# Kernel tuning notes

Measured on AMD Instinct MI355X. Metric: run time of the kernel, lower is better.

The kernel has to match this reference:

```python
import jax, jax.numpy as jnp
import numpy as np

B, S, D_IN, E, H = 2, 2048, 1024, 1024, 16  # batch, seq, input_size, embedding_size, heads


def setup_inputs() -> dict:
    key = jax.random.key(0)
    k1, k2, k3 = jax.random.split(key, 3)
    x = jax.random.normal(k1, (B, S, D_IN), dtype=jnp.float32)
    # fused QKV projection weight stored as [in, 3E] (torch Linear weight transposed)
    W0 = jax.random.normal(k2, (D_IN, 3 * E), dtype=jnp.float32) * (1.0 / np.sqrt(D_IN))
    b0 = jax.random.normal(k3, (3 * E,), dtype=jnp.float32) * 0.02
    return {"x": x, "W0": W0, "b0": b0}


def reference(x, W0, b0):
    b, s, _ = x.shape
    y = x @ W0 + b0                              # [B,S,3E]
    y = y.reshape(b, s, H, -1).transpose(0, 2, 1, 3)  # [B,H,S,3*head_dim]
    q, k, v = jnp.split(y, 3, axis=-1)           # each [B,H,S,head_dim]
    scale = 1.0 / jnp.sqrt(jnp.asarray(D_IN, dtype=x.dtype))  # NB: sqrt(input_size), as in source
    scores = jnp.einsum("bhqd,bhkd->bhqk", q, k) * scale
    # causal mask: -inf above diagonal
    causal = jnp.triu(jnp.full((s, s), -jnp.inf, dtype=scores.dtype), k=1)
    scores = scores + causal
    attn = jax.nn.softmax(scores, axis=-1)       # [B,H,S,S]
    o = jnp.einsum("bhqk,bhkd->bhqd", attn, v)   # [B,H,S,head_dim]
    # faithful to source: reshape directly from (B,H,S,d) to (B,S,H*d) WITHOUT permuting back
    return o.reshape(b, s, -1)
```

## Files before the change

### kernel.cpp

```cpp
#include <hip/hip_runtime.h>
#include <stdint.h>

typedef __attribute__((ext_vector_type(4))) float f32x4;
typedef __attribute__((ext_vector_type(16))) float f32x16;
typedef __attribute__((ext_vector_type(8))) short bf16x8;
typedef __attribute__((ext_vector_type(4))) short bf16x4;

#define MFMA16(a, b, c) __builtin_amdgcn_mfma_f32_16x16x32_bf16((a), (b), (c), 0, 0, 0)
#define MFMA32(a, b, c) __builtin_amdgcn_mfma_f32_32x32x16_bf16((a), (b), (c), 0, 0, 0)

__device__ __forceinline__ short f2bf(float f) {
    union { float f; uint32_t u; } v; v.f = f;
    uint32_t r = (v.u + 0x7fffu + ((v.u >> 16) & 1u)) >> 16;
    return (short)(uint16_t)r;
}
__device__ __forceinline__ float bf2f(short s) {
    union { uint32_t u; float f; } v; v.u = ((uint32_t)(uint16_t)s) << 16;
    return v.f;
}
__device__ __forceinline__ float fast_exp2(float x) {
    float r; asm("v_exp_f32 %0, %1" : "=v"(r) : "v"(x)); return r;
}

__device__ __forceinline__ void async_ld16(const short* g, short* l) {
    __builtin_amdgcn_global_load_lds(
        (const __attribute__((address_space(1))) uint32_t*)g,
        (__attribute__((address_space(3))) uint32_t*)l, 16, 0, 0);
}

#define MK_BFRAG(C, O, OUT) do {                                                   \
    uint32_t a_, b_, c_, d_;                                                       \
    asm("v_cvt_pk_bf16_f32 %0, %1, %2" : "=v"(a_) : "v"((C)[(O)+0]), "v"((C)[(O)+1])); \
    asm("v_cvt_pk_bf16_f32 %0, %1, %2" : "=v"(c_) : "v"((C)[(O)+2]), "v"((C)[(O)+3])); \
    asm("v_cvt_pk_bf16_f32 %0, %1, %2" : "=v"(b_) : "v"((C)[(O)+4]), "v"((C)[(O)+5])); \
    asm("v_cvt_pk_bf16_f32 %0, %1, %2" : "=v"(d_) : "v"((C)[(O)+6]), "v"((C)[(O)+7])); \
    asm("v_permlane32_swap_b32 %0, %1" : "+v"(a_), "+v"(b_));                      \
    asm("v_permlane32_swap_b32 %0, %1" : "+v"(c_), "+v"(d_));                      \
    union { uint32_t u[4]; bf16x8 v; } pb_;                                        \
    pb_.u[0] = a_; pb_.u[1] = c_; pb_.u[2] = b_; pb_.u[3] = d_;                    \
    OUT = pb_.v;                                                                   \
} while (0)

__global__ __launch_bounds__(256)
void convert_fused(const float* __restrict__ X, short* __restrict__ Xb,
                   const float* __restrict__ W, short* __restrict__ Wt) {
    __shared__ short T[64][72];
    const int t = threadIdx.x;
    const int id = blockIdx.x;
    if (id < 2048) {
        const int i8 = (id * 256 + t) << 3;
        f32x4 a = *(const f32x4*)(X + i8);
        f32x4 b = *(const f32x4*)(X + i8 + 4);
        bf16x8 o;
#pragma unroll
        for (int j = 0; j < 4; ++j) { o[j] = f2bf(a[j]); o[4 + j] = f2bf(b[j]); }
        *(bf16x8*)(Xb + i8) = o;
        return;
    }
    const int wid = id - 2048;
    const int n0 = (wid % 48) * 64, k0 = (wid / 48) * 64;
#pragma unroll
    for (int i = 0; i < 4; ++i) {
        const int r = i * 16 + (t >> 4);
        const int c = (t & 15) << 2;
        f32x4 v = *(const f32x4*)(W + (size_t)(k0 + r) * 3072 + n0 + c);
#pragma unroll
        for (int j = 0; j < 4; ++j) T[c + j][r] = f2bf(v[j]);
    }
    __syncthreads();
#pragma unroll
    for (int i = 0; i < 2; ++i) {
        const int r = i * 32 + (t >> 3);
        const int c = (t & 7) << 3;
        *(bf16x8*)(Wt + (size_t)(n0 + r) * 1024 + k0 + c) = *(const bf16x8*)&T[r][c];
    }
}

__global__ __launch_bounds__(256, 3)
void gemm_pack(const short* __restrict__ Xb, const short* __restrict__ Wt,
               const float* __restrict__ bias, short* __restrict__ Qp,
               short* __restrict__ Kp, short* __restrict__ Vp) {
    __shared__ short Asm[3][128 * 32];
    __shared__ short Bsm[3][128 * 32];

    const int tid  = threadIdx.x;
    const int lane = tid & 63;
    const int l15  = lane & 15;
    const int lq   = lane >> 4;
    const int wave = tid >> 6;
    const int wr = wave >> 1, wc = wave & 1;

    const int bid = blockIdx.x;
    const int swz = (bid & 7) * 96 + (bid >> 3);
    const int m0 = (swz / 24) * 128, n0 = (swz % 24) * 128;

    const int srow = tid >> 2;
    const int scolsw = (((tid & 3) ^ (srow & 3)) << 3);

    f32x4 acc[4][4];
#pragma unroll
    for (int m = 0; m < 4; ++m)
#pragma unroll
        for (int n = 0; n < 4; ++n) acc[m][n] = (f32x4)(0.0f);

    auto stage = [&](int k0, int bb) {
#pragma unroll
        for (int i = 0; i < 2; ++i)
            async_ld16(Xb + (size_t)(m0 + i * 64 + srow) * 1024 + k0 + scolsw,
                       &Asm[bb][(i * 256 + wave * 64) * 8]);
#pragma unroll
        for (int i = 0; i < 2; ++i)
            async_ld16(Wt + (size_t)(n0 + i * 64 + srow) * 1024 + k0 + scolsw,
                       &Bsm[bb][(i * 256 + wave * 64) * 8]);
    };

    const int gsw = ((lq ^ (l15 & 3)) << 3);

    auto compute = [&](int bb) {
        bf16x8 af[4], bfv[4];
#pragma unroll
        for (int m = 0; m < 4; ++m)
            af[m] = *(const bf16x8*)&Asm[bb][(wr * 64 + m * 16 + l15) * 32 + gsw];
#pragma unroll
        for (int n = 0; n < 4; ++n)
            bfv[n] = *(const bf16x8*)&Bsm[bb][(wc * 64 + n * 16 + l15) * 32 + gsw];
#pragma unroll
        for (int m = 0; m < 4; ++m)
#pragma unroll
            for (int n = 0; n < 4; ++n) acc[m][n] = MFMA16(af[m], bfv[n], acc[m][n]);
    };

#define WAITV(N) do {                                           \
        asm volatile("s_waitcnt vmcnt(" #N ")" ::: "memory");   \
        __builtin_amdgcn_sched_barrier(0);                      \
        __builtin_amdgcn_s_barrier();                           \
        __builtin_amdgcn_sched_barrier(0);                      \
    } while (0)

    stage(0, 0);
    stage(32, 1);
#pragma unroll 1
    for (int kt = 0; kt < 30; ++kt) {
        WAITV(4);
        compute(kt % 3);
        stage((kt + 2) * 32, (kt + 2) % 3);
    }
    WAITV(4);
    compute(0);
    WAITV(0);
    compute(1);
#undef WAITV

    const float SCALE2 = 0.03125f * 1.44269504f;
    float bv[4];
#pragma unroll
    for (int n = 0; n < 4; ++n) bv[n] = bias[n0 + wc * 64 + n * 16 + l15];

    const size_t bbase = (size_t)(m0 >> 11) * 2097152;
    const int tokb = (m0 & 2047) + wr * 64;

#pragma unroll
    for (int n = 0; n < 4; ++n) {
        const int col = n0 + wc * 64 + n * 16 + l15;
        const int h   = col / 192;
        const int seg = (col >> 6) % 3;
        const int d   = col & 63;
        const size_t hb = bbase + (size_t)h * 131072;
        if (seg == 0) {
            const int cp = ((d >> 4) << 9) + (((d >> 3) & 1) << 8) + (d & 7);
#pragma unroll
            for (int m = 0; m < 4; ++m)
#pragma unroll
                for (int r = 0; r < 4; ++r) {
                    const int tok = tokb + m * 16 + (lq << 2) + r;
                    Qp[hb + ((size_t)(tok >> 5) << 11) + ((tok & 31) << 3) + cp] =
                        f2bf((acc[m][n][r] + bv[n]) * SCALE2);
                }
        } else if (seg == 1) {
            const int cp = ((d >> 4) << 10) + (((d >> 3) & 1) << 8) + (d & 7);
#pragma unroll
            for (int m = 0; m < 4; ++m)
#pragma unroll
                for (int r = 0; r < 4; ++r) {
                    const int tok = tokb + m * 16 + (lq << 2) + r;
                    Kp[hb + ((size_t)(tok >> 6) << 12) + (((tok >> 5) & 1) << 9)
                       + ((tok & 31) << 3) + cp] = f2bf(acc[m][n][r] + bv[n]);
                }
        } else {
            const int cp = ((d >> 5) << 11) + ((d & 31) << 3);
#pragma unroll
            for (int m = 0; m < 4; ++m)
#pragma unroll
                for (int r = 0; r < 4; ++r) {
                    const int tok = tokb + m * 16 + (lq << 2) + r;
                    Vp[hb + ((size_t)(tok >> 6) << 12) + (((tok >> 4) & 3) << 9)
                       + (((tok >> 3) & 1) << 8) + (tok & 7) + cp] =
                        f2bf(acc[m][n][r] + bv[n]);
                }
        }
    }
}

__global__ __launch_bounds__(64, 3)
void attn_part(const short* __restrict__ Qp, const short* __restrict__ Kp,
               const short* __restrict__ Vp, short* __restrict__ Po,
               float* __restrict__ Pm) {
    const int tid = threadIdx.x;
    const int l31 = tid & 31;
    const int hi  = tid >> 5;

    const int id  = blockIdx.x;
    const int xcd = id & 7;
    const int idx = id >> 3;
    const int u   = idx >> 2;
    const int bh  = xcd * 4 + (idx & 3);

    int qt, t0, t1;
    bool hasDiag;
    if (u < 32) {
        qt = u + 32; t0 = 0; t1 = 16; hasDiag = false;
    } else {
        const int s = 16 - ((u - 32) >> 2);
        const int j = (u - 32) & 3;
        if (j < 2) { qt = 2 * s - 2 + j;       t0 = 0;  t1 = s; }
        else       { qt = 2 * s + 30 + (j - 2); t0 = 16; t1 = s + 16; }
        hasDiag = true;
    }
    const int q0 = qt * 32;

    const size_t hb = (size_t)bh * 131072;

    bf16x8 qf[4];
    {
        const short* qp = Qp + hb + qt * 2048 + tid * 8;
#pragma unroll
        for (int dg = 0; dg < 4; ++dg) qf[dg] = *(const bf16x8*)(qp + dg * 512);
    }

    f32x16 o0 = (f32x16)(0.f), o1 = (f32x16)(0.f);
    float m_run = -1e30f, l_run = 0.f;
    const int qg = q0 + l31;

    bf16x8 kA[8], kB[8], va[8];

    auto loadK = [&](bf16x8 (&kr)[8], int t) {
        const short* p = Kp + hb + (size_t)t * 4096 + tid * 8;
#pragma unroll
        for (int f = 0; f < 8; ++f)
            kr[f] = *(const bf16x8*)(p + (f >> 1) * 1024 + (f & 1) * 512);
    };
    auto loadV = [&](int t) {
        const short* p = Vp + hb + (size_t)t * 4096 + tid * 8;
#pragma unroll
        for (int f = 0; f < 8; ++f) va[f] = *(const bf16x8*)(p + f * 512);
    };
    auto qk = [&](bf16x8 (&kr)[8], f32x16& c0, f32x16& c1) {
#pragma unroll
        for (int dg = 0; dg < 4; ++dg) {
            c0 = MFMA32(kr[2 * dg],     qf[dg], c0);
            c1 = MFMA32(kr[2 * dg + 1], qf[dg], c1);
        }
    };

    auto smpv = [&](f32x16& c0, f32x16& c1, int kv0, bool DIAG) {
        if (DIAG) {
#pragma unroll
            for (int r = 0; r < 16; ++r) {
                const int kvr = kv0 + (r & 3) + 8 * (r >> 2) + 4 * hi;
                if (kvr > qg)      c0[r] = -1e30f;
                if (kvr + 32 > qg) c1[r] = -1e30f;
            }
        }

        float mr[8];
#pragma unroll
        for (int r = 0; r < 8; ++r)
            mr[r] = fmaxf(fmaxf(c0[r], c0[8 + r]), fmaxf(c1[r], c1[8 + r]));
        float mx = fmaxf(fmaxf(fmaxf(mr[0], mr[1]), fmaxf(mr[2], mr[3])),
                         fmaxf(fmaxf(mr[4], mr[5]), fmaxf(mr[6], mr[7])));
        mx = fmaxf(mx, __shfl_xor(mx, 32, 64));

        if (!__all(mx <= m_run + 8.f)) {
            const float mnew = fmaxf(m_run, mx);
            const float corr = fast_exp2(m_run - mnew);
            l_run *= corr;
            o0 = o0 * corr;
            o1 = o1 * corr;
            m_run = mnew;
        }

        float ps0 = 0.f, ps1 = 0.f, ps2 = 0.f, ps3 = 0.f;
#pragma unroll
        for (int r = 0; r < 4; ++r) {
            c0[r]      = fast_exp2(c0[r]      - m_run); ps0 += c0[r];
            c0[4 + r]  = fast_exp2(c0[4 + r]  - m_run); ps1 += c0[4 + r];
            c0[8 + r]  = fast_exp2(c0[8 + r]  - m_run); ps2 += c0[8 + r];
            c0[12 + r] = fast_exp2(c0[12 + r] - m_run); ps3 += c0[12 + r];
        }
#pragma unroll
        for (int r = 0; r < 4; ++r) {
            c1[r]      = fast_exp2(c1[r]      - m_run); ps0 += c1[r];
            c1[4 + r]  = fast_exp2(c1[4 + r]  - m_run); ps1 += c1[4 + r];
            c1[8 + r]  = fast_exp2(c1[8 + r]  - m_run); ps2 += c1[8 + r];
            c1[12 + r] = fast_exp2(c1[12 + r] - m_run); ps3 += c1[12 + r];
        }
        l_run += (ps0 + ps1) + (ps2 + ps3);

        bf16x8 bf00, bf01, bf10, bf11;
        MK_BFRAG(c0, 0, bf00);
        MK_BFRAG(c0, 8, bf01);
        MK_BFRAG(c1, 0, bf10);
        MK_BFRAG(c1, 8, bf11);

        o0 = MFMA32(va[0], bf00, o0);
        o0 = MFMA32(va[1], bf01, o0);
        o0 = MFMA32(va[2], bf10, o0);
        o0 = MFMA32(va[3], bf11, o0);
        o1 = MFMA32(va[4], bf00, o1);
        o1 = MFMA32(va[5], bf01, o1);
        o1 = MFMA32(va[6], bf10, o1);
        o1 = MFMA32(va[7], bf11, o1);
    };

    int t = t0;
    loadK(kA, t0);
#pragma unroll 1
    for (; t + 2 < t1; t += 2) {
        f32x16 c0 = (f32x16)(0.f), c1 = (f32x16)(0.f);
        qk(kA, c0, c1);
        loadK(kB, t + 1);
        loadV(t);
        smpv(c0, c1, t * 64, false);
        f32x16 d0 = (f32x16)(0.f), d1 = (f32x16)(0.f);
        qk(kB, d0, d1);
        loadK(kA, t + 2);
        loadV(t + 1);
        smpv(d0, d1, (t + 1) * 64, false);
    }
    if (t + 1 < t1) {
        f32x16 c0 = (f32x16)(0.f), c1 = (f32x16)(0.f);
        qk(kA, c0, c1);
        loadK(kB, t + 1);
        loadV(t);
        smpv(c0, c1, t * 64, false);
        f32x16 d0 = (f32x16)(0.f), d1 = (f32x16)(0.f);
        qk(kB, d0, d1);
        loadV(t + 1);
        smpv(d0, d1, (t + 1) * 64, hasDiag);
    } else {
        f32x16 c0 = (f32x16)(0.f), c1 = (f32x16)(0.f);
        qk(kA, c0, c1);
        loadV(t);
        smpv(c0, c1, t * 64, hasDiag);
    }

    const float l_tot = l_run + __shfl_xor(l_run, 32, 64);
    const float inv = 1.f / l_tot;
    const int prow = (bh * 96 + u) * 32 + l31;
#pragma unroll
    for (int g = 0; g < 4; ++g) {
        bf16x4 w4;
#pragma unroll
        for (int j = 0; j < 4; ++j) w4[j] = f2bf(o0[g * 4 + j] * inv);
        *(bf16x4*)&Po[(size_t)prow * 64 + 8 * g + 4 * hi] = w4;
#pragma unroll
        for (int j = 0; j < 4; ++j) w4[j] = f2bf(o1[g * 4 + j] * inv);
        *(bf16x4*)&Po[(size_t)prow * 64 + 32 + 4 * hi + 8 * g] = w4;
    }
    if (hi == 0) Pm[prow] = m_run + __log2f(l_tot);
}

__global__ __launch_bounds__(256)
void attn_combine(const short* __restrict__ Po, const float* __restrict__ Pm,
                  float* __restrict__ Out) {
    const int idx = blockIdx.x * 256 + threadIdx.x;
    const int d4 = (idx & 15) << 2;
    const int rg = idx >> 4;
    const int q  = rg & 2047;
    const int bh = rg >> 11;
    const int qt = q >> 5, r = q & 31;

    f32x4 ov;
    if (qt < 32) {
        const int s = (qt >> 1) + 1;
        const int u = 32 + (16 - s) * 4 + (qt & 1);
        const int p0 = (bh * 96 + u) * 32 + r;
        bf16x4 a = *(const bf16x4*)&Po[(size_t)p0 * 64 + d4];
#pragma unroll
        for (int j = 0; j < 4; ++j) ov[j] = bf2f(a[j]);
    } else {
        const int u0 = qt - 32;
        const int s  = (qt >> 1) - 15;
        const int u1 = 32 + (16 - s) * 4 + 2 + (qt & 1);
        const int p0 = (bh * 96 + u0) * 32 + r;
        const int p1 = (bh * 96 + u1) * 32 + r;
        bf16x4 a = *(const bf16x4*)&Po[(size_t)p0 * 64 + d4];
        bf16x4 c = *(const bf16x4*)&Po[(size_t)p1 * 64 + d4];
        const float m0 = Pm[p0], m1 = Pm[p1];
        const float M = fmaxf(m0, m1);
        const float w0 = exp2f(m0 - M), w1 = exp2f(m1 - M);
        const float inv = 1.f / (w0 + w1);
#pragma unroll
        for (int j = 0; j < 4; ++j) ov[j] = (w0 * bf2f(a[j]) + w1 * bf2f(c[j])) * inv;
    }
    *(f32x4*)&Out[(size_t)rg * 64 + d4] = ov;
}

extern "C" void kernel_launch(void* const* d_in, const int* in_sizes, int n_in,
                              void* d_out, int out_size, void* d_ws, size_t ws_size,
                              hipStream_t stream) {
    const float* x  = (const float*)d_in[0];
    const float* W0 = (const float*)d_in[1];
    const float* b0 = (const float*)d_in[2];
    float* out = (float*)d_out;
    char* ws = (char*)d_ws;

    const size_t SEG_B = (size_t)32 * 131072 * 2;
    const size_t QKV_B = 3 * SEG_B;
    const size_t XBF_B = (size_t)4096 * 1024 * 2;
    const size_t PO_B  = (size_t)32 * 96 * 32 * 64 * 2;

    short* qp = (short*)ws;
    short* kp = (short*)(ws + SEG_B);
    short* vp = (short*)(ws + 2 * SEG_B);
    short* xb = (short*)(ws + QKV_B);
    short* wt = (short*)(ws + QKV_B + XBF_B);
    short* po = (short*)(ws + QKV_B);
    float* pm = (float*)(ws + QKV_B + PO_B);

    convert_fused<<<dim3(2816), dim3(256), 0, stream>>>(x, xb, W0, wt);
    gemm_pack<<<dim3(768), dim3(256), 0, stream>>>(xb, wt, b0, qp, kp, vp);
    attn_part<<<dim3(3072), dim3(64), 0, stream>>>(qp, kp, vp, po, pm);
    attn_combine<<<dim3(4096), dim3(256), 0, stream>>>(po, pm, out);
}
```

Before: 87.64 us.

## Split attention KV loop across four waves with LDS softmax merge

Each attention block now runs four wavefronts instead of one. The waves take interleaved KV tiles (stride 4), and their partial outputs and max/sum statistics are merged through shared memory with a log-sum-exp rescale by wave 0. The goal is to cut per-block serial latency over the KV loop and raise the number of in-flight waves. In exchange it adds a barrier, LDS traffic and combine arithmetic. Waves with no tiles sit idle for short diagonal tiles, and the register budget under launch bounds 256 may tighten.

Measured after the change: 147.8 us. +68.6%, slower.

```diff
diff --git a/kernel.cpp b/kernel.cpp
--- a/kernel.cpp
+++ b/kernel.cpp
@@ -201,13 +201,18 @@
     }
 }
 
-__global__ __launch_bounds__(64, 3)
+__global__ __launch_bounds__(256, 3)
 void attn_part(const short* __restrict__ Qp, const short* __restrict__ Kp,
                const short* __restrict__ Vp, short* __restrict__ Po,
                float* __restrict__ Pm) {
-    const int tid = threadIdx.x;
-    const int l31 = tid & 31;
-    const int hi  = tid >> 5;
+    __shared__ float oX[3][32 * 65];
+    __shared__ float lmX[3][64];
+
+    const int tid  = threadIdx.x;
+    const int lane = tid & 63;
+    const int l31  = tid & 31;
+    const int hi   = (tid >> 5) & 1;
+    const int w    = tid >> 6;
 
     const int id  = blockIdx.x;
     const int xcd = id & 7;
@@ -216,23 +221,22 @@
     const int bh  = xcd * 4 + (idx & 3);
 
     int qt, t0, t1;
-    bool hasDiag;
     if (u < 32) {
-        qt = u + 32; t0 = 0; t1 = 16; hasDiag = false;
+        qt = u + 32; t0 = 0; t1 = 16;
     } else {
         const int s = 16 - ((u - 32) >> 2);
         const int j = (u - 32) & 3;
-        if (j < 2) { qt = 2 * s - 2 + j;       t0 = 0;  t1 = s; }
+        if (j < 2) { qt = 2 * s - 2 + j;        t0 = 0;  t1 = s; }
         else       { qt = 2 * s + 30 + (j - 2); t0 = 16; t1 = s + 16; }
-        hasDiag = true;
     }
     const int q0 = qt * 32;
+    const int dt = qt >> 1;
 
     const size_t hb = (size_t)bh * 131072;
 
     bf16x8 qf[4];
     {
-        const short* qp = Qp + hb + qt * 2048 + tid * 8;
+        const short* qp = Qp + hb + qt * 2048 + lane * 8;
 #pragma unroll
         for (int dg = 0; dg < 4; ++dg) qf[dg] = *(const bf16x8*)(qp + dg * 512);
     }
@@ -244,13 +248,13 @@
     bf16x8 kA[8], kB[8], va[8];
 
     auto loadK = [&](bf16x8 (&kr)[8], int t) {
-        const short* p = Kp + hb + (size_t)t * 4096 + tid * 8;
+        const short* p = Kp + hb + (size_t)t * 4096 + lane * 8;
 #pragma unroll
         for (int f = 0; f < 8; ++f)
             kr[f] = *(const bf16x8*)(p + (f >> 1) * 1024 + (f & 1) * 512);
     };
     auto loadV = [&](int t) {
-        const short* p = Vp + hb + (size_t)t * 4096 + tid * 8;
+        const short* p = Vp + hb + (size_t)t * 4096 + lane * 8;
 #pragma unroll
         for (int f = 0; f < 8; ++f) va[f] = *(const bf16x8*)(p + f * 512);
     };
@@ -322,52 +326,102 @@
         o1 = MFMA32(va[7], bf11, o1);
     };
 
-    int t = t0;
-    loadK(kA, t0);
+    int t = t0 + w;
+    if (t < t1) {
+        loadK(kA, t);
 #pragma unroll 1
-    for (; t + 2 < t1; t += 2) {
-        f32x16 c0 = (f32x16)(0.f), c1 = (f32x16)(0.f);
-        qk(kA, c0, c1);
-        loadK(kB, t + 1);
-        loadV(t);
-        smpv(c0, c1, t * 64, false);
-        f32x16 d0 = (f32x16)(0.f), d1 = (f32x16)(0.f);
-        qk(kB, d0, d1);
-        loadK(kA, t + 2);
-        loadV(t + 1);
-        smpv(d0, d1, (t + 1) * 64, false);
-    }
-    if (t + 1 < t1) {
-        f32x16 c0 = (f32x16)(0.f), c1 = (f32x16)(0.f);
-        qk(kA, c0, c1);
-        loadK(kB, t + 1);
-        loadV(t);
-        smpv(c0, c1, t * 64, false);
-        f32x16 d0 = (f32x16)(0.f), d1 = (f32x16)(0.f);
-        qk(kB, d0, d1);
-        loadV(t + 1);
-        smpv(d0, d1, (t + 1) * 64, hasDiag);
-    } else {
-        f32x16 c0 = (f32x16)(0.f), c1 = (f32x16)(0.f);
-        qk(kA, c0, c1);
-        loadV(t);
-        smpv(c0, c1, t * 64, hasDiag);
+        while (t + 8 < t1) {
+            f32x16 c0 = (f32x16)(0.f), c1 = (f32x16)(0.f);
+            qk(kA, c0, c1);
+            loadK(kB, t + 4);
+            loadV(t);
+            smpv(c0, c1, t * 64, t == dt);
+            f32x16 d0 = (f32x16)(0.f), d1 = (f32x16)(0.f);
+            qk(kB, d0, d1);
+            loadK(kA, t + 8);
+            loadV(t + 4);
+            smpv(d0, d1, (t + 4) * 64, (t + 4) == dt);
+            t += 8;
+        }
+        if (t + 4 < t1) {
+            f32x16 c0 = (f32x16)(0.f), c1 = (f32x16)(0.f);
+            qk(kA, c0, c1);
+            loadK(kB, t + 4);
+            loadV(t);
+            smpv(c0, c1, t * 64, t == dt);
+            f32x16 d0 = (f32x16)(0.f), d1 = (f32x16)(0.f);
+            qk(kB, d0, d1);
+            loadV(t + 4);
+            smpv(d0, d1, (t + 4) * 64, (t + 4) == dt);
+        } else {
+            f32x16 c0 = (f32x16)(0.f), c1 = (f32x16)(0.f);
+            qk(kA, c0, c1);
+            loadV(t);
+            smpv(c0, c1, t * 64, t == dt);
+        }
     }
 
     const float l_tot = l_run + __shfl_xor(l_run, 32, 64);
-    const float inv = 1.f / l_tot;
-    const int prow = (bh * 96 + u) * 32 + l31;
-#pragma unroll
-    for (int g = 0; g < 4; ++g) {
-        bf16x4 w4;
-#pragma unroll
-        for (int j = 0; j < 4; ++j) w4[j] = f2bf(o0[g * 4 + j] * inv);
-        *(bf16x4*)&Po[(size_t)prow * 64 + 8 * g + 4 * hi] = w4;
-#pragma unroll
-        for (int j = 0; j < 4; ++j) w4[j] = f2bf(o1[g * 4 + j] * inv);
-        *(bf16x4*)&Po[(size_t)prow * 64 + 32 + 4 * hi + 8 * g] = w4;
-    }
-    if (hi == 0) Pm[prow] = m_run + __log2f(l_tot);
+
+    if (w > 0) {
+        float* dst = &oX[w - 1][l31 * 65];
+#pragma unroll
+        for (int g = 0; g < 4; ++g) {
+            f32x4 v0, v1;
+#pragma unroll
+            for (int j = 0; j < 4; ++j) { v0[j] = o0[4 * g + j]; v1[j] = o1[4 * g + j]; }
+            *(f32x4*)&dst[8 * g + 4 * hi]      = v0;
+            *(f32x4*)&dst[32 + 8 * g + 4 * hi] = v1;
+        }
+        if (hi == 0) { lmX[w - 1][l31 * 2] = m_run; lmX[w - 1][l31 * 2 + 1] = l_tot; }
+    }
+    __syncthreads();
+
+    if (w == 0) {
+        float mw[3], lw[3];
+        float M = m_run;
+#pragma unroll
+        for (int i = 0; i < 3; ++i) {
+            mw[i] = lmX[i][l31 * 2];
+            lw[i] = lmX[i][l31 * 2 + 1];
+            M = fmaxf(M, mw[i]);
+        }
+        const float wt0 = fast_exp2(m_run - M);
+        float L = l_tot * wt0;
+        float wts[3];
+#pragma unroll
+        for (int i = 0; i < 3; ++i) { wts[i] = fast_exp2(mw[i] - M); L += lw[i] * wts[i]; }
+
+        f32x16 a0 = o0 * wt0, a1 = o1 * wt0;
+#pragma unroll
+        for (int i = 0; i < 3; ++i) {
+            const float* src = &oX[i][l31 * 65];
+#pragma unroll
+            for (int g = 0; g < 4; ++g) {
+                f32x4 v0 = *(const f32x4*)&src[8 * g + 4 * hi];
+                f32x4 v1 = *(const f32x4*)&src[32 + 8 * g + 4 * hi];
+#pragma unroll
+                for (int j = 0; j < 4; ++j) {
+                    a0[4 * g + j] += wts[i] * v0[j];
+                    a1[4 * g + j] += wts[i] * v1[j];
+                }
+            }
+        }
+
+        const float inv = 1.f / L;
+        const int prow = (bh * 96 + u) * 32 + l31;
+#pragma unroll
+        for (int g = 0; g < 4; ++g) {
+            bf16x4 w4;
+#pragma unroll
+            for (int j = 0; j < 4; ++j) w4[j] = f2bf(a0[g * 4 + j] * inv);
+            *(bf16x4*)&Po[(size_t)prow * 64 + 8 * g + 4 * hi] = w4;
+#pragma unroll
+            for (int j = 0; j < 4; ++j) w4[j] = f2bf(a1[g * 4 + j] * inv);
+            *(bf16x4*)&Po[(size_t)prow * 64 + 32 + 8 * g + 4 * hi] = w4;
+        }
+        if (hi == 0) Pm[prow] = M + __log2f(L);
+    }
 }
 
 __global__ __launch_bounds__(256)
@@ -430,6 +484,6 @@
 
     convert_fused<<<dim3(2816), dim3(256), 0, stream>>>(x, xb, W0, wt);
     gemm_pack<<<dim3(768), dim3(256), 0, stream>>>(xb, wt, b0, qp, kp, vp);
-    attn_part<<<dim3(3072), dim3(64), 0, stream>>>(qp, kp, vp, po, pm);
+    attn_part<<<dim3(3072), dim3(256), 0, stream>>>(qp, kp, vp, po, pm);
     attn_combine<<<dim3(4096), dim3(256), 0, stream>>>(po, pm, out);
 }
```
